# Performance work log

Measured on AMD Instinct MI355X. Metric: run time of the kernel, lower is better.

## Reference

```python
import jax, jax.numpy as jnp
import numpy as np

MASK_VALUE = -1e6


def setup_inputs() -> dict:
    key = jax.random.key(0)
    ks = jax.random.split(key, 8)
    B, Lq, Lk, D, H = 4, 512, 512, 128, 128
    return {
        "queries": jax.random.normal(ks[0], (B, Lq, D), dtype=jnp.float32),
        "keys": jax.random.normal(ks[1], (B, Lk, D), dtype=jnp.float32),
        "values": jax.random.normal(ks[2], (B, Lk, D), dtype=jnp.float32),
        "valid_seq_len": jax.random.randint(ks[3], (B,), 1, Lk + 1),
        "Wq": jax.random.normal(ks[4], (D, H), dtype=jnp.float32) * 0.05,
        "Wk": jax.random.normal(ks[5], (D, H), dtype=jnp.float32) * 0.05,
        "wv": jax.random.normal(ks[6], (H,), dtype=jnp.float32) * 0.05,
        "Wo": jax.random.normal(ks[7], (D, H), dtype=jnp.float32) * 0.05,
    }


def reference(queries, keys, values, valid_seq_len, Wq, Wk, wv, Wo):
    # q: (B,Lq,H), k: (B,Lk,H)
    q = jnp.einsum("bqd,dh->bqh", queries, Wq)
    k = jnp.einsum("bkd,dh->bkh", keys, Wk)
    # additive features: (B,Lq,Lk,H) -> scalar scores via wv
    feat = jnp.tanh(q[:, :, None, :] + k[:, None, :, :])
    scores = jnp.einsum("bqkh,h->bqk", feat, wv)
    # mask invalid key positions per batch (softmax over last dim)
    Lk = keys.shape[1]
    mask = jnp.arange(Lk)[None, None, :] < valid_seq_len[:, None, None]
    scores = jnp.where(mask, scores, MASK_VALUE)
    attn = jax.nn.softmax(scores, axis=-1)  # (B,Lq,Lk)
    out = jnp.einsum("bqk,bkd->bqd", attn, values)
    return jnp.einsum("bqd,dh->bqh", out, Wo)
```

## Files before the change

kernel.cpp:

```cpp
#include <hip/hip_runtime.h>
#include <hip/hip_bf16.h>

#define B_   4
#define LQ   512
#define LK   512
#define D_   128
#define H_   128
#define LKP  576
#define QSS  4
#define QSF  4

#define TWO_LOG2E 2.885390081777927f
#define LOG2E     1.442695040888963f

__device__ __forceinline__ float fexp2(float x) {
#if __has_builtin(__builtin_amdgcn_exp2f)
  return __builtin_amdgcn_exp2f(x);
#else
  return exp2f(x);
#endif
}
__device__ __forceinline__ float frcp(float x) {
#if __has_builtin(__builtin_amdgcn_rcpf)
  return __builtin_amdgcn_rcpf(x);
#else
  return __fdividef(1.0f, x);
#endif
}

__device__ __forceinline__ void sig4k(float eq, float w, float4 ek, float4& acc) {
  float d0 = fmaf(eq, ek.x, 1.f);
  float d1 = fmaf(eq, ek.y, 1.f);
  float d2 = fmaf(eq, ek.z, 1.f);
  float d3 = fmaf(eq, ek.w, 1.f);
  float R01 = frcp(d0 * d1);
  float R23 = frcp(d2 * d3);
  acc.x = fmaf(w * d1, R01, acc.x);
  acc.y = fmaf(w * d0, R01, acc.y);
  acc.z = fmaf(w * d3, R23, acc.z);
  acc.w = fmaf(w * d2, R23, acc.w);
}

__global__ __launch_bounds__(256) void proj_kernel(
    const float* __restrict__ queries, const float* __restrict__ keys,
    const float* __restrict__ Wq, const float* __restrict__ Wk,
    float* __restrict__ Eq, float* __restrict__ EkT) {
  __shared__ float s_x[8][D_];
  int r0 = blockIdx.x * 8;
  bool qside = r0 < B_ * LQ;
  const float* X = qside ? queries : keys;
  const float* W = qside ? Wq : Wk;
  int rb = qside ? r0 : r0 - B_ * LQ;
  int tid = threadIdx.x;
  for (int i = tid; i < 8 * D_; i += 256)
    s_x[i >> 7][i & 127] = X[(size_t)(rb + (i >> 7)) * D_ + (i & 127)];
  __syncthreads();
  int h = tid & 127, rh = tid >> 7;
  const float4* x0 = (const float4*)s_x[rh * 4 + 0];
  const float4* x1 = (const float4*)s_x[rh * 4 + 1];
  const float4* x2 = (const float4*)s_x[rh * 4 + 2];
  const float4* x3 = (const float4*)s_x[rh * 4 + 3];
  float a0 = 0.f, a1 = 0.f, a2 = 0.f, a3 = 0.f;
  #pragma unroll 8
  for (int d4 = 0; d4 < D_ / 4; ++d4) {
    float4 xa = x0[d4], xb = x1[d4], xc = x2[d4], xd = x3[d4];
    const float* Wd = W + 4 * d4 * H_ + h;
    float w0 = Wd[0], w1 = Wd[H_], w2 = Wd[2 * H_], w3 = Wd[3 * H_];
    a0 = fmaf(xa.x, w0, fmaf(xa.y, w1, fmaf(xa.z, w2, fmaf(xa.w, w3, a0))));
    a1 = fmaf(xb.x, w0, fmaf(xb.y, w1, fmaf(xb.z, w2, fmaf(xb.w, w3, a1))));
    a2 = fmaf(xc.x, w0, fmaf(xc.y, w1, fmaf(xc.z, w2, fmaf(xc.w, w3, a2))));
    a3 = fmaf(xd.x, w0, fmaf(xd.y, w1, fmaf(xd.z, w2, fmaf(xd.w, w3, a3))));
  }
  if (qside) {
    Eq[(size_t)(rb + rh * 4 + 0) * H_ + h] = fexp2(a0 * TWO_LOG2E);
    Eq[(size_t)(rb + rh * 4 + 1) * H_ + h] = fexp2(a1 * TWO_LOG2E);
    Eq[(size_t)(rb + rh * 4 + 2) * H_ + h] = fexp2(a2 * TWO_LOG2E);
    Eq[(size_t)(rb + rh * 4 + 3) * H_ + h] = fexp2(a3 * TWO_LOG2E);
  } else {
    int b = rb >> 9, kk = (rb & 511) + rh * 4;
    float* dst = EkT + ((size_t)b * H_ + h) * LKP + kk;
    dst[0] = fexp2(a0 * TWO_LOG2E);
    dst[1] = fexp2(a1 * TWO_LOG2E);
    dst[2] = fexp2(a2 * TWO_LOG2E);
    dst[3] = fexp2(a3 * TWO_LOG2E);
  }
}

__global__ __launch_bounds__(256) void score_kernel(
    const float* __restrict__ Eq, const float* __restrict__ EkT,
    const int* __restrict__ vlen_arr, const float* __restrict__ wv,
    float* __restrict__ sc_g) {
  int id = blockIdx.x;
  int b = id & 3, q0 = (id >> 2) * QSS;
  int tid = threadIdx.x;

  __shared__ float s_eq[QSS][H_];
  __shared__ float s_wv[H_];

  for (int i = tid; i < QSS * H_; i += 256)
    s_eq[i >> 7][i & 127] = Eq[(size_t)(b * LQ + q0 + (i >> 7)) * H_ + (i & 127)];
  if (tid < H_) s_wv[tid] = wv[tid];
  __syncthreads();
  int vlen = vlen_arr[b];

  const float4* wv4p = (const float4*)s_wv;
  float sum_wv = 0.f;
  #pragma unroll
  for (int j = 0; j < H_ / 4; ++j) {
    float4 t4 = wv4p[j];
    sum_wv += t4.x + t4.y + t4.z + t4.w;
  }

  int kq = tid & 127, rp = tid >> 7;
  int k0 = kq * 4;
  if (k0 < vlen) {
    const float4* ekp = (const float4*)(EkT + (size_t)b * H_ * LKP);
    const float4* qa4 = (const float4*)s_eq[2 * rp + 0];
    const float4* qb4 = (const float4*)s_eq[2 * rp + 1];
    float4 accA = {0.f, 0.f, 0.f, 0.f};
    float4 accB = {0.f, 0.f, 0.f, 0.f};
    #pragma unroll 2
    for (int h4 = 0; h4 < H_ / 4; ++h4) {
      float4 e0 = ekp[(size_t)(4 * h4 + 0) * (LKP / 4) + kq];
      float4 e1 = ekp[(size_t)(4 * h4 + 1) * (LKP / 4) + kq];
      float4 e2 = ekp[(size_t)(4 * h4 + 2) * (LKP / 4) + kq];
      float4 e3 = ekp[(size_t)(4 * h4 + 3) * (LKP / 4) + kq];
      float4 w4 = wv4p[h4];
      float4 qa = qa4[h4];
      float4 qb = qb4[h4];
      sig4k(qa.x, w4.x, e0, accA);  sig4k(qb.x, w4.x, e0, accB);
      sig4k(qa.y, w4.y, e1, accA);  sig4k(qb.y, w4.y, e1, accB);
      sig4k(qa.z, w4.z, e2, accA);  sig4k(qb.z, w4.z, e2, accB);
      sig4k(qa.w, w4.w, e3, accA);  sig4k(qb.w, w4.w, e3, accB);
    }
    float4 rA = { fmaf(-2.f, accA.x, sum_wv), fmaf(-2.f, accA.y, sum_wv),
                  fmaf(-2.f, accA.z, sum_wv), fmaf(-2.f, accA.w, sum_wv) };
    float4 rB = { fmaf(-2.f, accB.x, sum_wv), fmaf(-2.f, accB.y, sum_wv),
                  fmaf(-2.f, accB.z, sum_wv), fmaf(-2.f, accB.w, sum_wv) };
    ((float4*)(sc_g + (size_t)(b * LQ + q0 + 2 * rp + 0) * LK))[kq] = rA;
    ((float4*)(sc_g + (size_t)(b * LQ + q0 + 2 * rp + 1) * LK))[kq] = rB;
  }
}

__global__ __launch_bounds__(256) void finish_kernel(
    const float* __restrict__ sc_g, const float* __restrict__ values,
    const int* __restrict__ vlen_arr, const float* __restrict__ Wo,
    float* __restrict__ out) {
  int id = blockIdx.x;
  int b = id & 3, q0 = (id >> 2) * QSF;
  int tid = threadIdx.x, wave = tid >> 6, lane = tid & 63;
  int vlen = vlen_arr[b];

  __shared__ float s_w[QSF][LK];
  __shared__ float s_po[QSF][QSF][D_];
  __shared__ float s_pr[QSF][D_];

  {
    const float* srow = sc_g + (size_t)(b * LQ + q0 + wave) * LK;
    float vals[LK / 64];
    float m = -3.0e38f;
    #pragma unroll
    for (int j = 0; j < LK / 64; ++j) {
      int k = lane + j * 64;
      float v = (k < vlen) ? srow[k] : -1.0e30f;
      vals[j] = v;
      m = fmaxf(m, v);
    }
    #pragma unroll
    for (int off = 32; off; off >>= 1) m = fmaxf(m, __shfl_xor(m, off));
    float sum = 0.f;
    #pragma unroll
    for (int j = 0; j < LK / 64; ++j) {
      float e = fexp2((vals[j] - m) * LOG2E);
      vals[j] = e;
      sum += e;
    }
    #pragma unroll
    for (int off = 32; off; off >>= 1) sum += __shfl_xor(sum, off);
    float inv = frcp(sum);
    #pragma unroll
    for (int j = 0; j < LK / 64; ++j) s_w[wave][lane + j * 64] = vals[j] * inv;
  }
  __syncthreads();

  {
    int kbeg = wave * 128;
    int kend = min((vlen + 3) & ~3, kbeg + 128);
    const float4* v4 = (const float4*)(values + (size_t)b * LK * D_);
    int dq = lane & 31, kpar = lane >> 5;
    float4 a0 = {0,0,0,0}, a1 = {0,0,0,0}, a2 = {0,0,0,0}, a3 = {0,0,0,0};
    for (int kk = kbeg; kk < kend; kk += 4) {
      float4 va = v4[(size_t)(kk + 0 + kpar) * 32 + dq];
      float4 vb = v4[(size_t)(kk + 2 + kpar) * 32 + dq];
      float4 w0 = *(const float4*)&s_w[0][kk];
      float4 w1 = *(const float4*)&s_w[1][kk];
      float4 w2 = *(const float4*)&s_w[2][kk];
      float4 w3 = *(const float4*)&s_w[3][kk];
      float wa0 = kpar ? w0.y : w0.x, wb0 = kpar ? w0.w : w0.z;
      float wa1 = kpar ? w1.y : w1.x, wb1 = kpar ? w1.w : w1.z;
      float wa2 = kpar ? w2.y : w2.x, wb2 = kpar ? w2.w : w2.z;
      float wa3 = kpar ? w3.y : w3.x, wb3 = kpar ? w3.w : w3.z;
      a0.x = fmaf(wa0, va.x, fmaf(wb0, vb.x, a0.x));
      a0.y = fmaf(wa0, va.y, fmaf(wb0, vb.y, a0.y));
      a0.z = fmaf(wa0, va.z, fmaf(wb0, vb.z, a0.z));
      a0.w = fmaf(wa0, va.w, fmaf(wb0, vb.w, a0.w));
      a1.x = fmaf(wa1, va.x, fmaf(wb1, vb.x, a1.x));
      a1.y = fmaf(wa1, va.y, fmaf(wb1, vb.y, a1.y));
      a1.z = fmaf(wa1, va.z, fmaf(wb1, vb.z, a1.z));
      a1.w = fmaf(wa1, va.w, fmaf(wb1, vb.w, a1.w));
      a2.x = fmaf(wa2, va.x, fmaf(wb2, vb.x, a2.x));
      a2.y = fmaf(wa2, va.y, fmaf(wb2, vb.y, a2.y));
      a2.z = fmaf(wa2, va.z, fmaf(wb2, vb.z, a2.z));
      a2.w = fmaf(wa2, va.w, fmaf(wb2, vb.w, a2.w));
      a3.x = fmaf(wa3, va.x, fmaf(wb3, vb.x, a3.x));
      a3.y = fmaf(wa3, va.y, fmaf(wb3, vb.y, a3.y));
      a3.z = fmaf(wa3, va.z, fmaf(wb3, vb.z, a3.z));
      a3.w = fmaf(wa3, va.w, fmaf(wb3, vb.w, a3.w));
    }
    a0.x += __shfl_xor(a0.x, 32); a0.y += __shfl_xor(a0.y, 32);
    a0.z += __shfl_xor(a0.z, 32); a0.w += __shfl_xor(a0.w, 32);
    a1.x += __shfl_xor(a1.x, 32); a1.y += __shfl_xor(a1.y, 32);
    a1.z += __shfl_xor(a1.z, 32); a1.w += __shfl_xor(a1.w, 32);
    a2.x += __shfl_xor(a2.x, 32); a2.y += __shfl_xor(a2.y, 32);
    a2.z += __shfl_xor(a2.z, 32); a2.w += __shfl_xor(a2.w, 32);
    a3.x += __shfl_xor(a3.x, 32); a3.y += __shfl_xor(a3.y, 32);
    a3.z += __shfl_xor(a3.z, 32); a3.w += __shfl_xor(a3.w, 32);
    if (lane < 32) {
      ((float4*)s_po[wave][0])[dq] = a0;
      ((float4*)s_po[wave][1])[dq] = a1;
      ((float4*)s_po[wave][2])[dq] = a2;
      ((float4*)s_po[wave][3])[dq] = a3;
    }
  }
  __syncthreads();

  #pragma unroll
  for (int i = tid; i < QSF * D_; i += 256) {
    int r = i >> 7, d = i & 127;
    s_pr[r][d] = s_po[0][r][d] + s_po[1][r][d] + s_po[2][r][d] + s_po[3][r][d];
  }
  __syncthreads();

  {
    int h = tid & 127, r = tid >> 7;
    float accA = 0.f, accB = 0.f;
    #pragma unroll 8
    for (int d = 0; d < D_; ++d) {
      float w = Wo[d * H_ + h];
      accA = fmaf(s_pr[r][d], w, accA);
      accB = fmaf(s_pr[r + 2][d], w, accB);
    }
    out[(size_t)(b * LQ + q0 + r) * H_ + h] = accA;
    out[(size_t)(b * LQ + q0 + r + 2) * H_ + h] = accB;
  }
}

extern "C" void kernel_launch(void* const* d_in, const int* in_sizes, int n_in,
                              void* d_out, int out_size, void* d_ws, size_t ws_size,
                              hipStream_t stream) {
  const float* queries = (const float*)d_in[0];
  const float* keys    = (const float*)d_in[1];
  const float* values  = (const float*)d_in[2];
  const int*   vlen    = (const int*)d_in[3];
  const float* Wq      = (const float*)d_in[4];
  const float* Wk      = (const float*)d_in[5];
  const float* wv      = (const float*)d_in[6];
  const float* Wo      = (const float*)d_in[7];
  float* out = (float*)d_out;

  float* Eq   = (float*)d_ws;
  float* EkT  = Eq + (size_t)B_ * LQ * H_;
  float* sc_g = EkT + (size_t)B_ * H_ * LKP;

  proj_kernel<<<dim3(B_ * (LQ + LK) / 8), 256, 0, stream>>>(queries, keys, Wq, Wk, Eq, EkT);
  score_kernel<<<dim3(B_ * (LQ / QSS)), 256, 0, stream>>>(Eq, EkT, vlen, wv, sc_g);
  finish_kernel<<<dim3(B_ * (LQ / QSF)), 256, 0, stream>>>(sc_g, values, vlen, Wo, out);
}
```

Before: 126.0 us.

## Fuse score and softmax/output kernels into one kernel with shared-memory scores

Merges the score kernel and the finish kernel into a single fused kernel, so each block computes scores for two query rows, keeps them in shared memory, runs softmax, applies values and projects with Wo. This removes the global score buffer round trip and one kernel launch. Queries per block drop from four to two, which doubles the grid. As a trade-off, each EkT column and values row is reused across fewer queries, so more L2 traffic per query. Masking now happens when scores are written.

```diff
diff --git a/kernel.cpp b/kernel.cpp
--- a/kernel.cpp
+++ b/kernel.cpp
@@ -7,8 +7,7 @@
 #define D_   128
 #define H_   128
 #define LKP  576
-#define QSS  4
-#define QSF  4
+#define QS   2
 
 #define TWO_LOG2E 2.885390081777927f
 #define LOG2E     1.442695040888963f
@@ -86,19 +85,22 @@
   }
 }
 
-__global__ __launch_bounds__(256) void score_kernel(
+__global__ __launch_bounds__(256) void fused_kernel(
     const float* __restrict__ Eq, const float* __restrict__ EkT,
-    const int* __restrict__ vlen_arr, const float* __restrict__ wv,
-    float* __restrict__ sc_g) {
+    const float* __restrict__ values, const int* __restrict__ vlen_arr,
+    const float* __restrict__ wv, const float* __restrict__ Wo,
+    float* __restrict__ out) {
   int id = blockIdx.x;
-  int b = id & 3, q0 = (id >> 2) * QSS;
-  int tid = threadIdx.x;
-
-  __shared__ float s_eq[QSS][H_];
+  int b = id >> 8, q0 = (id & 255) * QS;
+  int tid = threadIdx.x, wave = tid >> 6, lane = tid & 63;
+
+  __shared__ float s_eq[QS][H_];
   __shared__ float s_wv[H_];
-
-  for (int i = tid; i < QSS * H_; i += 256)
-    s_eq[i >> 7][i & 127] = Eq[(size_t)(b * LQ + q0 + (i >> 7)) * H_ + (i & 127)];
+  __shared__ float s_sc[QS][LK];
+  __shared__ float s_po[4][QS][D_];
+  __shared__ float s_pr[QS][D_];
+
+  s_eq[tid >> 7][tid & 127] = Eq[(size_t)(b * LQ + q0 + (tid >> 7)) * H_ + (tid & 127)];
   if (tid < H_) s_wv[tid] = wv[tid];
   __syncthreads();
   int vlen = vlen_arr[b];
@@ -111,58 +113,45 @@
     sum_wv += t4.x + t4.y + t4.z + t4.w;
   }
 
-  int kq = tid & 127, rp = tid >> 7;
-  int k0 = kq * 4;
-  if (k0 < vlen) {
-    const float4* ekp = (const float4*)(EkT + (size_t)b * H_ * LKP);
-    const float4* qa4 = (const float4*)s_eq[2 * rp + 0];
-    const float4* qb4 = (const float4*)s_eq[2 * rp + 1];
-    float4 accA = {0.f, 0.f, 0.f, 0.f};
-    float4 accB = {0.f, 0.f, 0.f, 0.f};
-    #pragma unroll 2
-    for (int h4 = 0; h4 < H_ / 4; ++h4) {
-      float4 e0 = ekp[(size_t)(4 * h4 + 0) * (LKP / 4) + kq];
-      float4 e1 = ekp[(size_t)(4 * h4 + 1) * (LKP / 4) + kq];
-      float4 e2 = ekp[(size_t)(4 * h4 + 2) * (LKP / 4) + kq];
-      float4 e3 = ekp[(size_t)(4 * h4 + 3) * (LKP / 4) + kq];
-      float4 w4 = wv4p[h4];
-      float4 qa = qa4[h4];
-      float4 qb = qb4[h4];
-      sig4k(qa.x, w4.x, e0, accA);  sig4k(qb.x, w4.x, e0, accB);
-      sig4k(qa.y, w4.y, e1, accA);  sig4k(qb.y, w4.y, e1, accB);
-      sig4k(qa.z, w4.z, e2, accA);  sig4k(qb.z, w4.z, e2, accB);
-      sig4k(qa.w, w4.w, e3, accA);  sig4k(qb.w, w4.w, e3, accB);
-    }
-    float4 rA = { fmaf(-2.f, accA.x, sum_wv), fmaf(-2.f, accA.y, sum_wv),
-                  fmaf(-2.f, accA.z, sum_wv), fmaf(-2.f, accA.w, sum_wv) };
-    float4 rB = { fmaf(-2.f, accB.x, sum_wv), fmaf(-2.f, accB.y, sum_wv),
-                  fmaf(-2.f, accB.z, sum_wv), fmaf(-2.f, accB.w, sum_wv) };
-    ((float4*)(sc_g + (size_t)(b * LQ + q0 + 2 * rp + 0) * LK))[kq] = rA;
-    ((float4*)(sc_g + (size_t)(b * LQ + q0 + 2 * rp + 1) * LK))[kq] = rB;
-  }
-}
-
-__global__ __launch_bounds__(256) void finish_kernel(
-    const float* __restrict__ sc_g, const float* __restrict__ values,
-    const int* __restrict__ vlen_arr, const float* __restrict__ Wo,
-    float* __restrict__ out) {
-  int id = blockIdx.x;
-  int b = id & 3, q0 = (id >> 2) * QSF;
-  int tid = threadIdx.x, wave = tid >> 6, lane = tid & 63;
-  int vlen = vlen_arr[b];
-
-  __shared__ float s_w[QSF][LK];
-  __shared__ float s_po[QSF][QSF][D_];
-  __shared__ float s_pr[QSF][D_];
-
-  {
-    const float* srow = sc_g + (size_t)(b * LQ + q0 + wave) * LK;
+  {
+    int kq = tid & 127, rp = tid >> 7;
+    int k0 = kq * 4;
+    if (k0 < vlen) {
+      const float4* ekp = (const float4*)(EkT + (size_t)b * H_ * LKP);
+      const float4* eq4 = (const float4*)s_eq[rp];
+      float4 acc = {0.f, 0.f, 0.f, 0.f};
+      #pragma unroll 2
+      for (int h4 = 0; h4 < H_ / 4; ++h4) {
+        float4 e0 = ekp[(size_t)(4 * h4 + 0) * (LKP / 4) + kq];
+        float4 e1 = ekp[(size_t)(4 * h4 + 1) * (LKP / 4) + kq];
+        float4 e2 = ekp[(size_t)(4 * h4 + 2) * (LKP / 4) + kq];
+        float4 e3 = ekp[(size_t)(4 * h4 + 3) * (LKP / 4) + kq];
+        float4 w4 = wv4p[h4];
+        float4 q4 = eq4[h4];
+        sig4k(q4.x, w4.x, e0, acc);
+        sig4k(q4.y, w4.y, e1, acc);
+        sig4k(q4.z, w4.z, e2, acc);
+        sig4k(q4.w, w4.w, e3, acc);
+      }
+      float4 r;
+      r.x = fmaf(-2.f, acc.x, sum_wv);
+      r.y = (k0 + 1 < vlen) ? fmaf(-2.f, acc.y, sum_wv) : -1.0e6f;
+      r.z = (k0 + 2 < vlen) ? fmaf(-2.f, acc.z, sum_wv) : -1.0e6f;
+      r.w = (k0 + 3 < vlen) ? fmaf(-2.f, acc.w, sum_wv) : -1.0e6f;
+      ((float4*)s_sc[rp])[kq] = r;
+    } else {
+      float4 mm = {-1.0e6f, -1.0e6f, -1.0e6f, -1.0e6f};
+      ((float4*)s_sc[rp])[kq] = mm;
+    }
+  }
+  __syncthreads();
+
+  if (wave < QS) {
     float vals[LK / 64];
     float m = -3.0e38f;
     #pragma unroll
     for (int j = 0; j < LK / 64; ++j) {
-      int k = lane + j * 64;
-      float v = (k < vlen) ? srow[k] : -1.0e30f;
+      float v = s_sc[wave][lane + j * 64];
       vals[j] = v;
       m = fmaxf(m, v);
     }
@@ -179,7 +168,7 @@
     for (int off = 32; off; off >>= 1) sum += __shfl_xor(sum, off);
     float inv = frcp(sum);
     #pragma unroll
-    for (int j = 0; j < LK / 64; ++j) s_w[wave][lane + j * 64] = vals[j] * inv;
+    for (int j = 0; j < LK / 64; ++j) s_sc[wave][lane + j * 64] = vals[j] * inv;
   }
   __syncthreads();
 
@@ -188,18 +177,14 @@
     int kend = min((vlen + 3) & ~3, kbeg + 128);
     const float4* v4 = (const float4*)(values + (size_t)b * LK * D_);
     int dq = lane & 31, kpar = lane >> 5;
-    float4 a0 = {0,0,0,0}, a1 = {0,0,0,0}, a2 = {0,0,0,0}, a3 = {0,0,0,0};
+    float4 a0 = {0.f, 0.f, 0.f, 0.f}, a1 = {0.f, 0.f, 0.f, 0.f};
     for (int kk = kbeg; kk < kend; kk += 4) {
       float4 va = v4[(size_t)(kk + 0 + kpar) * 32 + dq];
       float4 vb = v4[(size_t)(kk + 2 + kpar) * 32 + dq];
-      float4 w0 = *(const float4*)&s_w[0][kk];
-      float4 w1 = *(const float4*)&s_w[1][kk];
-      float4 w2 = *(const float4*)&s_w[2][kk];
-      float4 w3 = *(const float4*)&s_w[3][kk];
+      float4 w0 = *(const float4*)&s_sc[0][kk];
+      float4 w1 = *(const float4*)&s_sc[1][kk];
       float wa0 = kpar ? w0.y : w0.x, wb0 = kpar ? w0.w : w0.z;
       float wa1 = kpar ? w1.y : w1.x, wb1 = kpar ? w1.w : w1.z;
-      float wa2 = kpar ? w2.y : w2.x, wb2 = kpar ? w2.w : w2.z;
-      float wa3 = kpar ? w3.y : w3.x, wb3 = kpar ? w3.w : w3.z;
       a0.x = fmaf(wa0, va.x, fmaf(wb0, vb.x, a0.x));
       a0.y = fmaf(wa0, va.y, fmaf(wb0, vb.y, a0.y));
       a0.z = fmaf(wa0, va.z, fmaf(wb0, vb.z, a0.z));
@@ -208,50 +193,31 @@
       a1.y = fmaf(wa1, va.y, fmaf(wb1, vb.y, a1.y));
       a1.z = fmaf(wa1, va.z, fmaf(wb1, vb.z, a1.z));
       a1.w = fmaf(wa1, va.w, fmaf(wb1, vb.w, a1.w));
-      a2.x = fmaf(wa2, va.x, fmaf(wb2, vb.x, a2.x));
-      a2.y = fmaf(wa2, va.y, fmaf(wb2, vb.y, a2.y));
-      a2.z = fmaf(wa2, va.z, fmaf(wb2, vb.z, a2.z));
-      a2.w = fmaf(wa2, va.w, fmaf(wb2, vb.w, a2.w));
-      a3.x = fmaf(wa3, va.x, fmaf(wb3, vb.x, a3.x));
-      a3.y = fmaf(wa3, va.y, fmaf(wb3, vb.y, a3.y));
-      a3.z = fmaf(wa3, va.z, fmaf(wb3, vb.z, a3.z));
-      a3.w = fmaf(wa3, va.w, fmaf(wb3, vb.w, a3.w));
     }
     a0.x += __shfl_xor(a0.x, 32); a0.y += __shfl_xor(a0.y, 32);
     a0.z += __shfl_xor(a0.z, 32); a0.w += __shfl_xor(a0.w, 32);
     a1.x += __shfl_xor(a1.x, 32); a1.y += __shfl_xor(a1.y, 32);
     a1.z += __shfl_xor(a1.z, 32); a1.w += __shfl_xor(a1.w, 32);
-    a2.x += __shfl_xor(a2.x, 32); a2.y += __shfl_xor(a2.y, 32);
-    a2.z += __shfl_xor(a2.z, 32); a2.w += __shfl_xor(a2.w, 32);
-    a3.x += __shfl_xor(a3.x, 32); a3.y += __shfl_xor(a3.y, 32);
-    a3.z += __shfl_xor(a3.z, 32); a3.w += __shfl_xor(a3.w, 32);
     if (lane < 32) {
       ((float4*)s_po[wave][0])[dq] = a0;
       ((float4*)s_po[wave][1])[dq] = a1;
-      ((float4*)s_po[wave][2])[dq] = a2;
-      ((float4*)s_po[wave][3])[dq] = a3;
-    }
-  }
-  __syncthreads();
-
-  #pragma unroll
-  for (int i = tid; i < QSF * D_; i += 256) {
-    int r = i >> 7, d = i & 127;
+    }
+  }
+  __syncthreads();
+
+  {
+    int r = tid >> 7, d = tid & 127;
     s_pr[r][d] = s_po[0][r][d] + s_po[1][r][d] + s_po[2][r][d] + s_po[3][r][d];
   }
   __syncthreads();
 
   {
     int h = tid & 127, r = tid >> 7;
-    float accA = 0.f, accB = 0.f;
+    float acc = 0.f;
     #pragma unroll 8
-    for (int d = 0; d < D_; ++d) {
-      float w = Wo[d * H_ + h];
-      accA = fmaf(s_pr[r][d], w, accA);
-      accB = fmaf(s_pr[r + 2][d], w, accB);
-    }
-    out[(size_t)(b * LQ + q0 + r) * H_ + h] = accA;
-    out[(size_t)(b * LQ + q0 + r + 2) * H_ + h] = accB;
+    for (int d = 0; d < D_; ++d)
+      acc = fmaf(s_pr[r][d], Wo[d * H_ + h], acc);
+    out[(size_t)(b * LQ + q0 + r) * H_ + h] = acc;
   }
 }
 
@@ -268,11 +234,9 @@
   const float* Wo      = (const float*)d_in[7];
   float* out = (float*)d_out;
 
-  float* Eq   = (float*)d_ws;
-  float* EkT  = Eq + (size_t)B_ * LQ * H_;
-  float* sc_g = EkT + (size_t)B_ * H_ * LKP;
+  float* Eq  = (float*)d_ws;
+  float* EkT = Eq + (size_t)B_ * LQ * H_;
 
   proj_kernel<<<dim3(B_ * (LQ + LK) / 8), 256, 0, stream>>>(queries, keys, Wq, Wk, Eq, EkT);
-  score_kernel<<<dim3(B_ * (LQ / QSS)), 256, 0, stream>>>(Eq, EkT, vlen, wv, sc_g);
-  finish_kernel<<<dim3(B_ * (LQ / QSF)), 256, 0, stream>>>(sc_g, values, vlen, Wo, out);
-}
+  fused_kernel<<<dim3(B_ * (LQ / QS)), 256, 0, stream>>>(Eq, EkT, values, vlen, wv, Wo, out);
+}
```

After: 118.1 us. -6.3%, faster.

## Fuse score and softmax/output kernels, keep scores in shared memory

Applied to the files above, without the earlier changes.

Merges the score kernel and the softmax/PV/output-projection kernel into one kernel that keeps the per-block score rows in LDS instead of writing them to a global scratch buffer. This removes a kernel launch and the global write/read of the full score matrix. The per-thread valid-length guard on score computation is removed, so scores for masked key positions are now computed and then discarded, which adds compute work for short sequences. It also raises LDS use per block.

```diff
diff --git a/kernel.cpp b/kernel.cpp
--- a/kernel.cpp
+++ b/kernel.cpp
@@ -7,8 +7,7 @@
 #define D_   128
 #define H_   128
 #define LKP  576
-#define QSS  4
-#define QSF  4
+#define QS   4
 
 #define TWO_LOG2E 2.885390081777927f
 #define LOG2E     1.442695040888963f
@@ -86,18 +85,22 @@
   }
 }
 
-__global__ __launch_bounds__(256) void score_kernel(
+__global__ __launch_bounds__(256) void fused_kernel(
     const float* __restrict__ Eq, const float* __restrict__ EkT,
-    const int* __restrict__ vlen_arr, const float* __restrict__ wv,
-    float* __restrict__ sc_g) {
+    const float* __restrict__ values, const int* __restrict__ vlen_arr,
+    const float* __restrict__ wv, const float* __restrict__ Wo,
+    float* __restrict__ out) {
   int id = blockIdx.x;
-  int b = id & 3, q0 = (id >> 2) * QSS;
-  int tid = threadIdx.x;
-
-  __shared__ float s_eq[QSS][H_];
+  int b = id & 3, q0 = (id >> 2) * QS;
+  int tid = threadIdx.x, wave = tid >> 6, lane = tid & 63;
+
+  __shared__ float s_eq[QS][H_];
   __shared__ float s_wv[H_];
-
-  for (int i = tid; i < QSS * H_; i += 256)
+  __shared__ float s_sc[QS][LK];
+  __shared__ float s_po[4][QS][D_];
+  __shared__ float s_pr[QS][D_];
+
+  for (int i = tid; i < QS * H_; i += 256)
     s_eq[i >> 7][i & 127] = Eq[(size_t)(b * LQ + q0 + (i >> 7)) * H_ + (i & 127)];
   if (tid < H_) s_wv[tid] = wv[tid];
   __syncthreads();
@@ -111,9 +114,8 @@
     sum_wv += t4.x + t4.y + t4.z + t4.w;
   }
 
-  int kq = tid & 127, rp = tid >> 7;
-  int k0 = kq * 4;
-  if (k0 < vlen) {
+  {
+    int kq = tid & 127, rp = tid >> 7;
     const float4* ekp = (const float4*)(EkT + (size_t)b * H_ * LKP);
     const float4* qa4 = (const float4*)s_eq[2 * rp + 0];
     const float4* qb4 = (const float4*)s_eq[2 * rp + 1];
@@ -137,32 +139,18 @@
                   fmaf(-2.f, accA.z, sum_wv), fmaf(-2.f, accA.w, sum_wv) };
     float4 rB = { fmaf(-2.f, accB.x, sum_wv), fmaf(-2.f, accB.y, sum_wv),
                   fmaf(-2.f, accB.z, sum_wv), fmaf(-2.f, accB.w, sum_wv) };
-    ((float4*)(sc_g + (size_t)(b * LQ + q0 + 2 * rp + 0) * LK))[kq] = rA;
-    ((float4*)(sc_g + (size_t)(b * LQ + q0 + 2 * rp + 1) * LK))[kq] = rB;
-  }
-}
-
-__global__ __launch_bounds__(256) void finish_kernel(
-    const float* __restrict__ sc_g, const float* __restrict__ values,
-    const int* __restrict__ vlen_arr, const float* __restrict__ Wo,
-    float* __restrict__ out) {
-  int id = blockIdx.x;
-  int b = id & 3, q0 = (id >> 2) * QSF;
-  int tid = threadIdx.x, wave = tid >> 6, lane = tid & 63;
-  int vlen = vlen_arr[b];
-
-  __shared__ float s_w[QSF][LK];
-  __shared__ float s_po[QSF][QSF][D_];
-  __shared__ float s_pr[QSF][D_];
-
-  {
-    const float* srow = sc_g + (size_t)(b * LQ + q0 + wave) * LK;
+    ((float4*)s_sc[2 * rp + 0])[kq] = rA;
+    ((float4*)s_sc[2 * rp + 1])[kq] = rB;
+  }
+  __syncthreads();
+
+  {
     float vals[LK / 64];
     float m = -3.0e38f;
     #pragma unroll
     for (int j = 0; j < LK / 64; ++j) {
       int k = lane + j * 64;
-      float v = (k < vlen) ? srow[k] : -1.0e30f;
+      float v = (k < vlen) ? s_sc[wave][k] : -1.0e30f;
       vals[j] = v;
       m = fmaxf(m, v);
     }
@@ -179,7 +167,7 @@
     for (int off = 32; off; off >>= 1) sum += __shfl_xor(sum, off);
     float inv = frcp(sum);
     #pragma unroll
-    for (int j = 0; j < LK / 64; ++j) s_w[wave][lane + j * 64] = vals[j] * inv;
+    for (int j = 0; j < LK / 64; ++j) s_sc[wave][lane + j * 64] = vals[j] * inv;
   }
   __syncthreads();
 
@@ -192,10 +180,10 @@
     for (int kk = kbeg; kk < kend; kk += 4) {
       float4 va = v4[(size_t)(kk + 0 + kpar) * 32 + dq];
       float4 vb = v4[(size_t)(kk + 2 + kpar) * 32 + dq];
-      float4 w0 = *(const float4*)&s_w[0][kk];
-      float4 w1 = *(const float4*)&s_w[1][kk];
-      float4 w2 = *(const float4*)&s_w[2][kk];
-      float4 w3 = *(const float4*)&s_w[3][kk];
+      float4 w0 = *(const float4*)&s_sc[0][kk];
+      float4 w1 = *(const float4*)&s_sc[1][kk];
+      float4 w2 = *(const float4*)&s_sc[2][kk];
+      float4 w3 = *(const float4*)&s_sc[3][kk];
       float wa0 = kpar ? w0.y : w0.x, wb0 = kpar ? w0.w : w0.z;
       float wa1 = kpar ? w1.y : w1.x, wb1 = kpar ? w1.w : w1.z;
       float wa2 = kpar ? w2.y : w2.x, wb2 = kpar ? w2.w : w2.z;
@@ -235,7 +223,7 @@
   __syncthreads();
 
   #pragma unroll
-  for (int i = tid; i < QSF * D_; i += 256) {
+  for (int i = tid; i < QS * D_; i += 256) {
     int r = i >> 7, d = i & 127;
     s_pr[r][d] = s_po[0][r][d] + s_po[1][r][d] + s_po[2][r][d] + s_po[3][r][d];
   }
@@ -268,11 +256,9 @@
   const float* Wo      = (const float*)d_in[7];
   float* out = (float*)d_out;
 
-  float* Eq   = (float*)d_ws;
-  float* EkT  = Eq + (size_t)B_ * LQ * H_;
-  float* sc_g = EkT + (size_t)B_ * H_ * LKP;
+  float* Eq  = (float*)d_ws;
+  float* EkT = Eq + (size_t)B_ * LQ * H_;
 
   proj_kernel<<<dim3(B_ * (LQ + LK) / 8), 256, 0, stream>>>(queries, keys, Wq, Wk, Eq, EkT);
-  score_kernel<<<dim3(B_ * (LQ / QSS)), 256, 0, stream>>>(Eq, EkT, vlen, wv, sc_g);
-  finish_kernel<<<dim3(B_ * (LQ / QSF)), 256, 0, stream>>>(sc_g, values, vlen, Wo, out);
-}
+  fused_kernel<<<dim3(B_ * (LQ / QS)), 256, 0, stream>>>(Eq, EkT, values, vlen, wv, Wo, out);
+}
```

After: 122.6 us. 2.7% less time.

## Split score kernel over key chunks and H halves, vectorize softmax loads

Applied to the files above, without the earlier changes.

The score kernel now partitions work across four key chunks and two halves of the hidden dimension, combining the partial sums through shared memory. This raises the block count from 512 to 2048 to improve occupancy and latency hiding. In exchange it drops the per-batch valid-length skip, so masked keys are computed too, and each EkT value is reused by only one query row per thread instead of two. The constant sum_wv term is removed, which is safe because softmax ignores a per-row constant. The softmax in the finish kernel now reads scores with float4 loads and writes weights with float4 stores.

```diff
diff --git a/kernel.cpp b/kernel.cpp
--- a/kernel.cpp
+++ b/kernel.cpp
@@ -7,8 +7,6 @@
 #define D_   128
 #define H_   128
 #define LKP  576
-#define QSS  4
-#define QSF  4
 
 #define TWO_LOG2E 2.885390081777927f
 #define LOG2E     1.442695040888963f
@@ -88,57 +86,49 @@
 
 __global__ __launch_bounds__(256) void score_kernel(
     const float* __restrict__ Eq, const float* __restrict__ EkT,
-    const int* __restrict__ vlen_arr, const float* __restrict__ wv,
-    float* __restrict__ sc_g) {
+    const float* __restrict__ wv, float* __restrict__ sc_g) {
   int id = blockIdx.x;
-  int b = id & 3, q0 = (id >> 2) * QSS;
+  int b = id & 3, kc = (id >> 2) & 3, qt = id >> 4;
+  int q0 = qt * 4;
   int tid = threadIdx.x;
 
-  __shared__ float s_eq[QSS][H_];
+  __shared__ float s_eq[4][H_];
   __shared__ float s_wv[H_];
-
-  for (int i = tid; i < QSS * H_; i += 256)
+  __shared__ float s_red[2][4][128];
+
+  for (int i = tid; i < 4 * H_; i += 256)
     s_eq[i >> 7][i & 127] = Eq[(size_t)(b * LQ + q0 + (i >> 7)) * H_ + (i & 127)];
   if (tid < H_) s_wv[tid] = wv[tid];
   __syncthreads();
-  int vlen = vlen_arr[b];
-
-  const float4* wv4p = (const float4*)s_wv;
-  float sum_wv = 0.f;
-  #pragma unroll
-  for (int j = 0; j < H_ / 4; ++j) {
-    float4 t4 = wv4p[j];
-    sum_wv += t4.x + t4.y + t4.z + t4.w;
-  }
-
-  int kq = tid & 127, rp = tid >> 7;
-  int k0 = kq * 4;
-  if (k0 < vlen) {
-    const float4* ekp = (const float4*)(EkT + (size_t)b * H_ * LKP);
-    const float4* qa4 = (const float4*)s_eq[2 * rp + 0];
-    const float4* qb4 = (const float4*)s_eq[2 * rp + 1];
-    float4 accA = {0.f, 0.f, 0.f, 0.f};
-    float4 accB = {0.f, 0.f, 0.f, 0.f};
-    #pragma unroll 2
-    for (int h4 = 0; h4 < H_ / 4; ++h4) {
-      float4 e0 = ekp[(size_t)(4 * h4 + 0) * (LKP / 4) + kq];
-      float4 e1 = ekp[(size_t)(4 * h4 + 1) * (LKP / 4) + kq];
-      float4 e2 = ekp[(size_t)(4 * h4 + 2) * (LKP / 4) + kq];
-      float4 e3 = ekp[(size_t)(4 * h4 + 3) * (LKP / 4) + kq];
-      float4 w4 = wv4p[h4];
-      float4 qa = qa4[h4];
-      float4 qb = qb4[h4];
-      sig4k(qa.x, w4.x, e0, accA);  sig4k(qb.x, w4.x, e0, accB);
-      sig4k(qa.y, w4.y, e1, accA);  sig4k(qb.y, w4.y, e1, accB);
-      sig4k(qa.z, w4.z, e2, accA);  sig4k(qb.z, w4.z, e2, accB);
-      sig4k(qa.w, w4.w, e3, accA);  sig4k(qb.w, w4.w, e3, accB);
-    }
-    float4 rA = { fmaf(-2.f, accA.x, sum_wv), fmaf(-2.f, accA.y, sum_wv),
-                  fmaf(-2.f, accA.z, sum_wv), fmaf(-2.f, accA.w, sum_wv) };
-    float4 rB = { fmaf(-2.f, accB.x, sum_wv), fmaf(-2.f, accB.y, sum_wv),
-                  fmaf(-2.f, accB.z, sum_wv), fmaf(-2.f, accB.w, sum_wv) };
-    ((float4*)(sc_g + (size_t)(b * LQ + q0 + 2 * rp + 0) * LK))[kq] = rA;
-    ((float4*)(sc_g + (size_t)(b * LQ + q0 + 2 * rp + 1) * LK))[kq] = rB;
+
+  int kq = tid & 31, row = (tid >> 5) & 3, hh = tid >> 7;
+  const float4* ekp = (const float4*)(EkT + (size_t)b * H_ * LKP);
+  int c = kc * 32 + kq;
+  const float* eqr = s_eq[row];
+  const float* wvp = s_wv;
+  int hbase = hh * 64;
+  float4 acc = {0.f, 0.f, 0.f, 0.f};
+  #pragma unroll 4
+  for (int h4 = 0; h4 < 16; ++h4) {
+    int h = hbase + h4 * 4;
+    float4 e0 = ekp[(size_t)(h + 0) * 144 + c];
+    float4 e1 = ekp[(size_t)(h + 1) * 144 + c];
+    float4 e2 = ekp[(size_t)(h + 2) * 144 + c];
+    float4 e3 = ekp[(size_t)(h + 3) * 144 + c];
+    sig4k(eqr[h + 0], wvp[h + 0], e0, acc);
+    sig4k(eqr[h + 1], wvp[h + 1], e1, acc);
+    sig4k(eqr[h + 2], wvp[h + 2], e2, acc);
+    sig4k(eqr[h + 3], wvp[h + 3], e3, acc);
+  }
+  ((float4*)s_red[hh][row])[kq] = acc;
+  __syncthreads();
+  if (tid < 128) {
+    int r2 = tid >> 5, k2 = tid & 31;
+    float4 a = ((const float4*)s_red[0][r2])[k2];
+    float4 b4 = ((const float4*)s_red[1][r2])[k2];
+    float4 r4 = { -2.f * (a.x + b4.x), -2.f * (a.y + b4.y),
+                  -2.f * (a.z + b4.z), -2.f * (a.w + b4.w) };
+    ((float4*)(sc_g + (size_t)(b * LQ + q0 + r2) * LK + kc * 128))[k2] = r4;
   }
 }
 
@@ -147,39 +137,44 @@
     const int* __restrict__ vlen_arr, const float* __restrict__ Wo,
     float* __restrict__ out) {
   int id = blockIdx.x;
-  int b = id & 3, q0 = (id >> 2) * QSF;
+  int b = id & 3, q0 = (id >> 2) * 4;
   int tid = threadIdx.x, wave = tid >> 6, lane = tid & 63;
   int vlen = vlen_arr[b];
 
-  __shared__ float s_w[QSF][LK];
-  __shared__ float s_po[QSF][QSF][D_];
-  __shared__ float s_pr[QSF][D_];
+  __shared__ float s_w[4][LK];
+  __shared__ float s_po[4][4][D_];
+  __shared__ float s_pr[4][D_];
 
   {
-    const float* srow = sc_g + (size_t)(b * LQ + q0 + wave) * LK;
-    float vals[LK / 64];
-    float m = -3.0e38f;
-    #pragma unroll
-    for (int j = 0; j < LK / 64; ++j) {
-      int k = lane + j * 64;
-      float v = (k < vlen) ? srow[k] : -1.0e30f;
-      vals[j] = v;
-      m = fmaxf(m, v);
-    }
+    const float4* srow4 = (const float4*)(sc_g + (size_t)(b * LQ + q0 + wave) * LK);
+    float4 v0 = srow4[lane];
+    float4 v1 = srow4[lane + 64];
+    int k0 = 4 * lane, k1 = 256 + 4 * lane;
+    v0.x = (k0 + 0 < vlen) ? v0.x : -1.0e30f;
+    v0.y = (k0 + 1 < vlen) ? v0.y : -1.0e30f;
+    v0.z = (k0 + 2 < vlen) ? v0.z : -1.0e30f;
+    v0.w = (k0 + 3 < vlen) ? v0.w : -1.0e30f;
+    v1.x = (k1 + 0 < vlen) ? v1.x : -1.0e30f;
+    v1.y = (k1 + 1 < vlen) ? v1.y : -1.0e30f;
+    v1.z = (k1 + 2 < vlen) ? v1.z : -1.0e30f;
+    v1.w = (k1 + 3 < vlen) ? v1.w : -1.0e30f;
+    float m = fmaxf(fmaxf(fmaxf(v0.x, v0.y), fmaxf(v0.z, v0.w)),
+                    fmaxf(fmaxf(v1.x, v1.y), fmaxf(v1.z, v1.w)));
     #pragma unroll
     for (int off = 32; off; off >>= 1) m = fmaxf(m, __shfl_xor(m, off));
-    float sum = 0.f;
-    #pragma unroll
-    for (int j = 0; j < LK / 64; ++j) {
-      float e = fexp2((vals[j] - m) * LOG2E);
-      vals[j] = e;
-      sum += e;
-    }
+    float4 e0, e1;
+    e0.x = fexp2((v0.x - m) * LOG2E);  e0.y = fexp2((v0.y - m) * LOG2E);
+    e0.z = fexp2((v0.z - m) * LOG2E);  e0.w = fexp2((v0.w - m) * LOG2E);
+    e1.x = fexp2((v1.x - m) * LOG2E);  e1.y = fexp2((v1.y - m) * LOG2E);
+    e1.z = fexp2((v1.z - m) * LOG2E);  e1.w = fexp2((v1.w - m) * LOG2E);
+    float sum = e0.x + e0.y + e0.z + e0.w + e1.x + e1.y + e1.z + e1.w;
     #pragma unroll
     for (int off = 32; off; off >>= 1) sum += __shfl_xor(sum, off);
     float inv = frcp(sum);
-    #pragma unroll
-    for (int j = 0; j < LK / 64; ++j) s_w[wave][lane + j * 64] = vals[j] * inv;
+    e0.x *= inv; e0.y *= inv; e0.z *= inv; e0.w *= inv;
+    e1.x *= inv; e1.y *= inv; e1.z *= inv; e1.w *= inv;
+    ((float4*)s_w[wave])[lane]      = e0;
+    ((float4*)s_w[wave])[lane + 64] = e1;
   }
   __syncthreads();
 
@@ -235,7 +230,7 @@
   __syncthreads();
 
   #pragma unroll
-  for (int i = tid; i < QSF * D_; i += 256) {
+  for (int i = tid; i < 4 * D_; i += 256) {
     int r = i >> 7, d = i & 127;
     s_pr[r][d] = s_po[0][r][d] + s_po[1][r][d] + s_po[2][r][d] + s_po[3][r][d];
   }
@@ -273,6 +268,6 @@
   float* sc_g = EkT + (size_t)B_ * H_ * LKP;
 
   proj_kernel<<<dim3(B_ * (LQ + LK) / 8), 256, 0, stream>>>(queries, keys, Wq, Wk, Eq, EkT);
-  score_kernel<<<dim3(B_ * (LQ / QSS)), 256, 0, stream>>>(Eq, EkT, vlen, wv, sc_g);
-  finish_kernel<<<dim3(B_ * (LQ / QSF)), 256, 0, stream>>>(sc_g, values, vlen, Wo, out);
-}
+  score_kernel<<<dim3(2048), 256, 0, stream>>>(Eq, EkT, wv, sc_g);
+  finish_kernel<<<dim3(512), 256, 0, stream>>>(sc_g, values, vlen, Wo, out);
+}
```

After: 114.1 us. 9.5% less time.
